# Kernel tuning notes

Measured on AMD Instinct MI355X. Metric: run time of the kernel, lower is better.

Reference implementation:

```python
import jax, jax.numpy as jnp
import numpy as np

N_NODES = 100000
NUM_LAYER = 3
REG_WEIGHT = 1e-4


def setup_inputs() -> dict:
    key = jax.random.key(0)
    ks = jax.random.split(key, 6)
    E = 1280000
    B = 4096
    D = 64
    # xavier-uniform-like scale for embedding table
    emb_weight = jax.random.normal(ks[0], (N_NODES, D), dtype=jnp.float32) * 0.01
    src = jax.random.randint(ks[1], (E,), 0, N_NODES, dtype=jnp.int32)
    dst = jax.random.randint(ks[2], (E,), 0, N_NODES, dtype=jnp.int32)
    users = jax.random.randint(ks[3], (B,), 0, N_NODES, dtype=jnp.int32)
    pos = jax.random.randint(ks[4], (B,), 0, N_NODES, dtype=jnp.int32)
    neg = jax.random.randint(ks[5], (B,), 0, N_NODES, dtype=jnp.int32)
    return {"emb_weight": emb_weight, "src": src, "dst": dst,
            "users": users, "pos": pos, "neg": neg}


def _edge_norm(src, dst):
    # DGL norm(): d = sum of edge mask (ones) per dst node; adj_e = d[src]^-0.5 * d[dst]^-0.5
    ones = jnp.ones(src.shape[0], dtype=jnp.float32)
    deg = jax.ops.segment_sum(ones, dst, num_segments=N_NODES)
    dinv = jnp.where(deg > 0, deg ** -0.5, 0.0)  # inf -> 0 handling
    return dinv[src] * dinv[dst]  # [E]


def _propagate(emb_weight, src, dst, adj):
    # LightGCN propagation: h_{l+1}[v] = sum_{(u->v)} adj_e * h_l[u]
    h = emb_weight
    layers = [h]
    for _ in range(NUM_LAYER):
        m = h[src] * adj[:, None]                    # [E, D] gather + edge weight
        h = jax.ops.segment_sum(m, dst, num_segments=N_NODES)  # [N, D] scatter-sum
        layers.append(h)
    return jnp.mean(jnp.stack(layers, axis=1), axis=1)  # mean over L+1 layers


def reference(emb_weight, src, dst, users, pos, neg):
    adj = _edge_norm(src, dst)
    all_emb = _propagate(emb_weight, src, dst, adj)

    u_e, p_e, n_e = all_emb[users], all_emb[pos], all_emb[neg]
    u0, p0, n0 = emb_weight[users], emb_weight[pos], emb_weight[neg]

    B = users.shape[0]
    reg_loss = 0.5 * (jnp.sum(u0 ** 2) + jnp.sum(p0 ** 2) + jnp.sum(n0 ** 2)) / B
    reg_loss = reg_loss * REG_WEIGHT

    pos_scores = jnp.sum(u_e * p_e, axis=1)
    neg_scores = jnp.sum(u_e * n_e, axis=1)
    loss_emb = jnp.mean(jax.nn.softplus(neg_scores - pos_scores))

    loss = loss_emb + reg_loss
    return loss, loss_emb, reg_loss
```

## Files before the change

### kernel.cpp

```cpp
#include <hip/hip_runtime.h>
#include <hip/hip_fp8.h>
#include <math.h>

#define N_NODES 100000
#define DIM 64
#define NUM_LAYER 3
#define BATCH 4096
#define REG_WEIGHT 1e-4f
#define NBUCKET 391
#define STAGE_CAP 4096
#define CURPAD 16
#define H_SCALE 64.0f
#define H_INV_SCALE (1.0f / 64.0f)

typedef float floatx2 __attribute__((ext_vector_type(2)));

__device__ unsigned char g_hf8[2][(size_t)N_NODES * DIM];
__device__ float g_sums[(size_t)3 * BATCH * DIM];
__device__ int   g_row_ptr[N_NODES + 1];
__device__ float g_dinv[N_NODES];
__device__ int   g_bcur[NBUCKET * CURPAD];
__device__ unsigned int g_stage[NBUCKET * STAGE_CAP];
__device__ int   g_csr[1280000];
__device__ int   g_shead[N_NODES];
__device__ int   g_snext[3 * BATCH];
__device__ float g_part_sp[BATCH];
__device__ float g_part_rg[BATCH];

__device__ inline void fma4_fp8(unsigned int d, float w,
                                float& a0, float& a1, float& a2, float& a3) {
    floatx2 lo = __builtin_amdgcn_cvt_pk_f32_fp8((int)d, false);
    floatx2 hi = __builtin_amdgcn_cvt_pk_f32_fp8((int)d, true);
    a0 = fmaf(w, lo.x, a0); a1 = fmaf(w, lo.y, a1);
    a2 = fmaf(w, hi.x, a2); a3 = fmaf(w, hi.y, a3);
}
__device__ inline unsigned int pack4_fp8(float a0, float a1, float a2, float a3) {
    int w = __builtin_amdgcn_cvt_pk_fp8_f32(a0, a1, 0, false);
    w     = __builtin_amdgcn_cvt_pk_fp8_f32(a2, a3, w, true);
    return (unsigned int)w;
}

#define EDGES_PER_THREAD 8
__global__ void __launch_bounds__(1024) stage_buckets(const int* __restrict__ src,
                                                      const int* __restrict__ dst, int E,
                                                      const int* __restrict__ users,
                                                      const int* __restrict__ pos,
                                                      const int* __restrict__ neg,
                                                      const float* __restrict__ emb) {
    __shared__ int h[NBUCKET];
    __shared__ int cur[NBUCKET];
    int tid = threadIdx.x;
    int gt = blockIdx.x * 1024 + tid;
    if (gt < 3 * BATCH) {
        int which = gt / BATCH, s = gt - which * BATCH;
        const int* idx = (which == 0) ? users : ((which == 1) ? pos : neg);
        g_snext[gt] = atomicExch(&g_shead[idx[s]], gt + 1);
    }
    int base = blockIdx.x * (1024 * EDGES_PER_THREAD);
    for (int i = tid; i < NBUCKET; i += 1024) h[i] = 0;
    __syncthreads();
    int myd[EDGES_PER_THREAD], mys[EDGES_PER_THREAD];
    #pragma unroll
    for (int k = 0; k < EDGES_PER_THREAD; ++k) {
        int e = base + k * 1024 + tid;
        if (e < E) {
            myd[k] = dst[e]; mys[k] = src[e];
            atomicAdd(&h[myd[k] >> 8], 1);
        } else myd[k] = -1;
    }
    __syncthreads();
    for (int i = tid; i < NBUCKET; i += 1024) {
        int c = h[i];
        cur[i] = c ? (atomicAdd(&g_bcur[i * CURPAD], c) + i * STAGE_CAP) : 0;
    }
    __syncthreads();
    #pragma unroll
    for (int k = 0; k < EDGES_PER_THREAD; ++k) {
        if (myd[k] >= 0) {
            int p = atomicAdd(&cur[myd[k] >> 8], 1);
            g_stage[p] = (unsigned int)((mys[k] << 8) | (myd[k] & 255));
        }
    }
    {
        const int NW = N_NODES * DIM / 4;
        int stride = gridDim.x * 1024;
        unsigned int* hw = (unsigned int*)g_hf8[0];
        for (int k = blockIdx.x * 1024 + tid; k < NW; k += stride) {
            const float* e = emb + (size_t)k * 4;
            hw[k] = pack4_fp8(e[0] * H_SCALE, e[1] * H_SCALE,
                              e[2] * H_SCALE, e[3] * H_SCALE);
        }
    }
}

__global__ void __launch_bounds__(512) finalize_place() {
    __shared__ int cs[512];
    __shared__ int lh[256], sc[256], cur[256];
    int b = blockIdx.x, t = threadIdx.x;
    int c = (t < NBUCKET) ? g_bcur[t * CURPAD] : 0;
    cs[t] = c;
    __syncthreads();
    for (int off = 1; off < 512; off <<= 1) {
        int x = (t >= off) ? cs[t - off] : 0;
        __syncthreads();
        cs[t] += x;
        __syncthreads();
    }
    int mybase = (b > 0) ? cs[b - 1] : 0;
    int cnt    = cs[b] - mybase;
    if (b == 0 && t == 0) g_row_ptr[N_NODES] = cs[NBUCKET - 1];
    int sbeg = b * STAGE_CAP;
    if (t < 256) lh[t] = 0;
    __syncthreads();
    for (int k = t; k < cnt; k += 512)
        atomicAdd(&lh[g_stage[sbeg + k] & 255], 1);
    __syncthreads();
    int v = 0;
    if (t < 256) { v = lh[t]; sc[t] = v; }
    __syncthreads();
    for (int off = 1; off < 256; off <<= 1) {
        int x = (t >= off && t < 256) ? sc[t - off] : 0;
        __syncthreads();
        if (t < 256) sc[t] += x;
        __syncthreads();
    }
    if (t < 256) {
        int start = mybase + sc[t] - v;
        cur[t] = start;
        int node = (b << 8) + t;
        if (node < N_NODES) {
            g_row_ptr[node] = start;
            g_dinv[node]    = (v > 0) ? rsqrtf((float)v) : 0.0f;
        }
    }
    __syncthreads();
    for (int k = t; k < cnt; k += 512) {
        unsigned int e = g_stage[sbeg + k];
        int pos = atomicAdd(&cur[e & 255], 1);
        g_csr[pos] = (int)(e >> 8);
    }
}

__global__ void pull_layer_fp8(const unsigned char* __restrict__ h,
                               unsigned char* __restrict__ hn, int do_gather) {
    int gid0 = blockIdx.x * blockDim.x + threadIdx.x;
    if (do_gather && gid0 < NBUCKET) g_bcur[gid0 * CURPAD] = 0;
    int wid  = gid0 >> 6;
    int lane = threadIdx.x & 63;
    int nA = wid * 2, nB = nA + 1;
    if (nA >= N_NODES) return;
    bool hasB = (nB < N_NODES);
    int g  = lane >> 4;
    int li = lane & 15;
    int begA = g_row_ptr[nA], endA = g_row_ptr[nA + 1];
    int begB = hasB ? g_row_ptr[nB] : 0, endB = hasB ? g_row_ptr[nB + 1] : 0;
    float dinvA = g_dinv[nA];
    float dinvB = hasB ? g_dinv[nB] : 0.0f;
    int lenA = endA - begA, lenB = endB - begB;
    int maxLen = max(lenA, lenB);
    float aA0 = 0.f, aA1 = 0.f, aA2 = 0.f, aA3 = 0.f;
    float aB0 = 0.f, aB1 = 0.f, aB2 = 0.f, aB3 = 0.f;
    for (int off = 0; off < maxLen; off += 64) {
        int kA = off + lane;
        int sA = 0; float wA = 0.0f;
        if (kA < lenA) { sA = g_csr[begA + kA]; wA = g_dinv[sA] * dinvA; }
        int sB = 0; float wB = 0.0f;
        if (kA < lenB) { sB = g_csr[begB + kA]; wB = g_dinv[sB] * dinvB; }
        int cnt = min(64, maxLen - off);
        for (int j = 0; j < cnt; j += 16) {
            int   sA1 = __shfl(sA, j + g),      sA2 = __shfl(sA, j + 4 + g);
            int   sA3 = __shfl(sA, j + 8 + g),  sA4 = __shfl(sA, j + 12 + g);
            int   sB1 = __shfl(sB, j + g),      sB2 = __shfl(sB, j + 4 + g);
            int   sB3 = __shfl(sB, j + 8 + g),  sB4 = __shfl(sB, j + 12 + g);
            float wA1 = __shfl(wA, j + g),      wA2 = __shfl(wA, j + 4 + g);
            float wA3 = __shfl(wA, j + 8 + g),  wA4 = __shfl(wA, j + 12 + g);
            float wB1 = __shfl(wB, j + g),      wB2 = __shfl(wB, j + 4 + g);
            float wB3 = __shfl(wB, j + 8 + g),  wB4 = __shfl(wB, j + 12 + g);
            unsigned int dA1 = *(const unsigned int*)(h + (size_t)sA1 * DIM + li * 4);
            unsigned int dA2 = *(const unsigned int*)(h + (size_t)sA2 * DIM + li * 4);
            unsigned int dA3 = *(const unsigned int*)(h + (size_t)sA3 * DIM + li * 4);
            unsigned int dA4 = *(const unsigned int*)(h + (size_t)sA4 * DIM + li * 4);
            unsigned int dB1 = *(const unsigned int*)(h + (size_t)sB1 * DIM + li * 4);
            unsigned int dB2 = *(const unsigned int*)(h + (size_t)sB2 * DIM + li * 4);
            unsigned int dB3 = *(const unsigned int*)(h + (size_t)sB3 * DIM + li * 4);
            unsigned int dB4 = *(const unsigned int*)(h + (size_t)sB4 * DIM + li * 4);
            fma4_fp8(dA1, wA1, aA0, aA1, aA2, aA3);
            fma4_fp8(dA2, wA2, aA0, aA1, aA2, aA3);
            fma4_fp8(dA3, wA3, aA0, aA1, aA2, aA3);
            fma4_fp8(dA4, wA4, aA0, aA1, aA2, aA3);
            fma4_fp8(dB1, wB1, aB0, aB1, aB2, aB3);
            fma4_fp8(dB2, wB2, aB0, aB1, aB2, aB3);
            fma4_fp8(dB3, wB3, aB0, aB1, aB2, aB3);
            fma4_fp8(dB4, wB4, aB0, aB1, aB2, aB3);
        }
    }
    #pragma unroll
    for (int off = 16; off < 64; off <<= 1) {
        aA0 += __shfl_xor(aA0, off); aA1 += __shfl_xor(aA1, off);
        aA2 += __shfl_xor(aA2, off); aA3 += __shfl_xor(aA3, off);
        aB0 += __shfl_xor(aB0, off); aB1 += __shfl_xor(aB1, off);
        aB2 += __shfl_xor(aB2, off); aB3 += __shfl_xor(aB3, off);
    }
    if (lane < 16) {
        *(unsigned int*)(hn + (size_t)nA * DIM + li * 4) = pack4_fp8(aA0, aA1, aA2, aA3);
        if (hasB)
            *(unsigned int*)(hn + (size_t)nB * DIM + li * 4) = pack4_fp8(aB0, aB1, aB2, aB3);
    }
    if (do_gather) {
        int sidx = g_shead[nA];
        while (sidx > 0) {
            int sreal = sidx - 1;
            if (lane < 16) {
                float* sp = &g_sums[(size_t)sreal * DIM + li * 4];
                sp[0] = aA0 * H_INV_SCALE; sp[1] = aA1 * H_INV_SCALE;
                sp[2] = aA2 * H_INV_SCALE; sp[3] = aA3 * H_INV_SCALE;
            }
            sidx = g_snext[sreal];
        }
        if (lane == 0) g_shead[nA] = 0;
        if (hasB) {
            sidx = g_shead[nB];
            while (sidx > 0) {
                int sreal = sidx - 1;
                if (lane < 16) {
                    float* sp = &g_sums[(size_t)sreal * DIM + li * 4];
                    sp[0] = aB0 * H_INV_SCALE; sp[1] = aB1 * H_INV_SCALE;
                    sp[2] = aB2 * H_INV_SCALE; sp[3] = aB3 * H_INV_SCALE;
                }
                sidx = g_snext[sreal];
            }
            if (lane == 0) g_shead[nB] = 0;
        }
    }
}

__global__ void pull_sampled(const unsigned char* __restrict__ h,
                             const int* __restrict__ users, const int* __restrict__ pos,
                             const int* __restrict__ neg) {
    int wid  = (blockIdx.x * blockDim.x + threadIdx.x) >> 6;
    int lane = threadIdx.x & 63;
    if (wid >= 3 * BATCH) return;
    int which = wid / BATCH;
    int i     = wid - which * BATCH;
    const int* idx = (which == 0) ? users : ((which == 1) ? pos : neg);
    int node = idx[i];
    int g  = lane >> 4;
    int li = lane & 15;
    int beg = g_row_ptr[node], end = g_row_ptr[node + 1];
    float dinv_d = g_dinv[node];
    float a0 = 0.f, a1 = 0.f, a2 = 0.f, a3 = 0.f;
    for (int base = beg; base < end; base += 64) {
        int k = base + lane;
        int s = 0; float w = 0.0f;
        if (k < end) { s = g_csr[k]; w = g_dinv[s] * dinv_d; }
        int cnt = min(64, end - base);
        for (int j = 0; j < cnt; j += 16) {
            int   sA = __shfl(s, j + g),      sB = __shfl(s, j + 4 + g);
            int   sC = __shfl(s, j + 8 + g),  sD = __shfl(s, j + 12 + g);
            float wA = __shfl(w, j + g),      wB = __shfl(w, j + 4 + g);
            float wC = __shfl(w, j + 8 + g),  wD = __shfl(w, j + 12 + g);
            unsigned int dA = *(const unsigned int*)(h + (size_t)sA * DIM + li * 4);
            unsigned int dB = *(const unsigned int*)(h + (size_t)sB * DIM + li * 4);
            unsigned int dC = *(const unsigned int*)(h + (size_t)sC * DIM + li * 4);
            unsigned int dD = *(const unsigned int*)(h + (size_t)sD * DIM + li * 4);
            fma4_fp8(dA, wA, a0, a1, a2, a3);
            fma4_fp8(dB, wB, a0, a1, a2, a3);
            fma4_fp8(dC, wC, a0, a1, a2, a3);
            fma4_fp8(dD, wD, a0, a1, a2, a3);
        }
    }
    #pragma unroll
    for (int off = 16; off < 64; off <<= 1) {
        a0 += __shfl_xor(a0, off);
        a1 += __shfl_xor(a1, off);
        a2 += __shfl_xor(a2, off);
        a3 += __shfl_xor(a3, off);
    }
    if (lane < 16) {
        unsigned int dn = *(const unsigned int*)(h + (size_t)node * DIM + li * 4);
        floatx2 lo = __builtin_amdgcn_cvt_pk_f32_fp8((int)dn, false);
        floatx2 hi = __builtin_amdgcn_cvt_pk_f32_fp8((int)dn, true);
        float* sp = &g_sums[(size_t)wid * DIM + li * 4];
        sp[0] += (a0 + lo.x) * H_INV_SCALE;
        sp[1] += (a1 + lo.y) * H_INV_SCALE;
        sp[2] += (a2 + hi.x) * H_INV_SCALE;
        sp[3] += (a3 + hi.y) * H_INV_SCALE;
    }
}

__global__ void score_reduce(const float* __restrict__ emb,
                             const int* __restrict__ users, const int* __restrict__ pos,
                             const int* __restrict__ neg) {
    int wid  = (blockIdx.x * blockDim.x + threadIdx.x) >> 6;
    int lane = threadIdx.x & 63;
    if (wid >= BATCH) return;
    float u0 = emb[(size_t)users[wid] * DIM + lane];
    float p0 = emb[(size_t)pos[wid]   * DIM + lane];
    float n0 = emb[(size_t)neg[wid]   * DIM + lane];
    float u = 0.25f * (g_sums[(size_t)wid * DIM + lane] + u0);
    float p = 0.25f * (g_sums[(size_t)(BATCH + wid) * DIM + lane] + p0);
    float n = 0.25f * (g_sums[(size_t)(2 * BATCH + wid) * DIM + lane] + n0);
    float ps = u * p;
    float ns = u * n;
    float rg = u0 * u0 + p0 * p0 + n0 * n0;
    #pragma unroll
    for (int off = 32; off > 0; off >>= 1) {
        ps += __shfl_down(ps, off);
        ns += __shfl_down(ns, off);
        rg += __shfl_down(rg, off);
    }
    if (lane == 0) {
        float x  = ns - ps;
        float sp = fmaxf(x, 0.0f) + log1pf(expf(-fabsf(x)));
        g_part_sp[wid] = sp;
        g_part_rg[wid] = rg;
    }
}

__global__ void final_reduce(float* __restrict__ out) {
    __shared__ float s_sp[256], s_rg[256];
    int t = threadIdx.x;
    float sp = 0.0f, rg = 0.0f;
    for (int i = t; i < BATCH; i += 256) { sp += g_part_sp[i]; rg += g_part_rg[i]; }
    s_sp[t] = sp; s_rg[t] = rg;
    __syncthreads();
    for (int off = 128; off > 0; off >>= 1) {
        if (t < off) { s_sp[t] += s_sp[t + off]; s_rg[t] += s_rg[t + off]; }
        __syncthreads();
    }
    if (t == 0) {
        float loss_emb = s_sp[0] / (float)BATCH;
        float reg      = 0.5f * s_rg[0] / (float)BATCH * REG_WEIGHT;
        out[0] = loss_emb + reg;
        out[1] = loss_emb;
        out[2] = reg;
    }
}

extern "C" void kernel_launch(void* const* d_in, const int* in_sizes, int n_in,
                              void* d_out, int out_size, void* d_ws, size_t ws_size,
                              hipStream_t stream) {
    const float* emb   = (const float*)d_in[0];
    const int*   src   = (const int*)d_in[1];
    const int*   dst   = (const int*)d_in[2];
    const int*   users = (const int*)d_in[3];
    const int*   pos   = (const int*)d_in[4];
    const int*   neg   = (const int*)d_in[5];
    const int E = in_sizes[1];
    float* out = (float*)d_out;

    unsigned char* hf_a;  hipGetSymbolAddress((void**)&hf_a, HIP_SYMBOL(g_hf8));
    unsigned char* hf_b = hf_a + (size_t)N_NODES * DIM;

    const int STAGE_BLOCKS = (E + 1024 * EDGES_PER_THREAD - 1) / (1024 * EDGES_PER_THREAD);
    stage_buckets<<<STAGE_BLOCKS, 1024, 0, stream>>>(src, dst, E, users, pos, neg, emb);
    finalize_place<<<NBUCKET, 512, 0, stream>>>();

    const int NPAIR = (N_NODES + 1) / 2;
    const int PULL_BLOCKS = (NPAIR * 64 + 255) / 256;

    pull_layer_fp8<<<PULL_BLOCKS, 256, 0, stream>>>(hf_a, hf_b, 1);

    pull_layer_fp8<<<PULL_BLOCKS, 256, 0, stream>>>(hf_b, hf_a, 0);

    pull_sampled<<<(3 * BATCH * 64 + 255) / 256, 256, 0, stream>>>(hf_a, users, pos, neg);

    score_reduce<<<(BATCH * 64 + 255) / 256, 256, 0, stream>>>(emb, users, pos, neg);
    final_reduce<<<1, 256, 0, stream>>>(out);
}
```

Measured before the change: 192.6 us.

## Pack source index with dinv into CSR and assign one node per quarter-wave

Adds a pass that builds an int2 CSR holding each source index next to its degree-inverse-sqrt, so the pull kernels no longer make a dependent gather into g_dinv per edge. The pull kernels now give each 16-lane quarter-wave its own destination node and walk its edges four at a time, replacing the cooperative index load, shuffles and cross-group xor reduction. This cuts shuffle and reduction overhead and idle lanes for low-degree nodes. In exchange it costs an extra kernel launch, a 10 MB int2 array to write and read, and more sequential per-node edge loops that each load redundant clamped entries.

Result: faster. 187.4 us (-2.7%).

```diff
diff --git a/kernel.cpp b/kernel.cpp
--- a/kernel.cpp
+++ b/kernel.cpp
@@ -22,6 +22,7 @@
 __device__ int   g_bcur[NBUCKET * CURPAD];
 __device__ unsigned int g_stage[NBUCKET * STAGE_CAP];
 __device__ int   g_csr[1280000];
+__device__ int2  g_csr2[1280000];
 __device__ int   g_shead[N_NODES];
 __device__ int   g_snext[3 * BATCH];
 __device__ float g_part_sp[BATCH];
@@ -141,151 +142,108 @@
     }
 }
 
+__global__ void build_wcsr(int E) {
+    int i = blockIdx.x * blockDim.x + threadIdx.x;
+    if (i < E) {
+        int s = g_csr[i];
+        g_csr2[i] = make_int2(s, __float_as_int(g_dinv[s]));
+    }
+}
+
 __global__ void pull_layer_fp8(const unsigned char* __restrict__ h,
                                unsigned char* __restrict__ hn, int do_gather) {
     int gid0 = blockIdx.x * blockDim.x + threadIdx.x;
     if (do_gather && gid0 < NBUCKET) g_bcur[gid0 * CURPAD] = 0;
     int wid  = gid0 >> 6;
     int lane = threadIdx.x & 63;
-    int nA = wid * 2, nB = nA + 1;
-    if (nA >= N_NODES) return;
-    bool hasB = (nB < N_NODES);
     int g  = lane >> 4;
     int li = lane & 15;
-    int begA = g_row_ptr[nA], endA = g_row_ptr[nA + 1];
-    int begB = hasB ? g_row_ptr[nB] : 0, endB = hasB ? g_row_ptr[nB + 1] : 0;
-    float dinvA = g_dinv[nA];
-    float dinvB = hasB ? g_dinv[nB] : 0.0f;
-    int lenA = endA - begA, lenB = endB - begB;
-    int maxLen = max(lenA, lenB);
-    float aA0 = 0.f, aA1 = 0.f, aA2 = 0.f, aA3 = 0.f;
-    float aB0 = 0.f, aB1 = 0.f, aB2 = 0.f, aB3 = 0.f;
-    for (int off = 0; off < maxLen; off += 64) {
-        int kA = off + lane;
-        int sA = 0; float wA = 0.0f;
-        if (kA < lenA) { sA = g_csr[begA + kA]; wA = g_dinv[sA] * dinvA; }
-        int sB = 0; float wB = 0.0f;
-        if (kA < lenB) { sB = g_csr[begB + kA]; wB = g_dinv[sB] * dinvB; }
-        int cnt = min(64, maxLen - off);
-        for (int j = 0; j < cnt; j += 16) {
-            int   sA1 = __shfl(sA, j + g),      sA2 = __shfl(sA, j + 4 + g);
-            int   sA3 = __shfl(sA, j + 8 + g),  sA4 = __shfl(sA, j + 12 + g);
-            int   sB1 = __shfl(sB, j + g),      sB2 = __shfl(sB, j + 4 + g);
-            int   sB3 = __shfl(sB, j + 8 + g),  sB4 = __shfl(sB, j + 12 + g);
-            float wA1 = __shfl(wA, j + g),      wA2 = __shfl(wA, j + 4 + g);
-            float wA3 = __shfl(wA, j + 8 + g),  wA4 = __shfl(wA, j + 12 + g);
-            float wB1 = __shfl(wB, j + g),      wB2 = __shfl(wB, j + 4 + g);
-            float wB3 = __shfl(wB, j + 8 + g),  wB4 = __shfl(wB, j + 12 + g);
-            unsigned int dA1 = *(const unsigned int*)(h + (size_t)sA1 * DIM + li * 4);
-            unsigned int dA2 = *(const unsigned int*)(h + (size_t)sA2 * DIM + li * 4);
-            unsigned int dA3 = *(const unsigned int*)(h + (size_t)sA3 * DIM + li * 4);
-            unsigned int dA4 = *(const unsigned int*)(h + (size_t)sA4 * DIM + li * 4);
-            unsigned int dB1 = *(const unsigned int*)(h + (size_t)sB1 * DIM + li * 4);
-            unsigned int dB2 = *(const unsigned int*)(h + (size_t)sB2 * DIM + li * 4);
-            unsigned int dB3 = *(const unsigned int*)(h + (size_t)sB3 * DIM + li * 4);
-            unsigned int dB4 = *(const unsigned int*)(h + (size_t)sB4 * DIM + li * 4);
-            fma4_fp8(dA1, wA1, aA0, aA1, aA2, aA3);
-            fma4_fp8(dA2, wA2, aA0, aA1, aA2, aA3);
-            fma4_fp8(dA3, wA3, aA0, aA1, aA2, aA3);
-            fma4_fp8(dA4, wA4, aA0, aA1, aA2, aA3);
-            fma4_fp8(dB1, wB1, aB0, aB1, aB2, aB3);
-            fma4_fp8(dB2, wB2, aB0, aB1, aB2, aB3);
-            fma4_fp8(dB3, wB3, aB0, aB1, aB2, aB3);
-            fma4_fp8(dB4, wB4, aB0, aB1, aB2, aB3);
+    int n = wid * 4 + g;
+    if (n >= N_NODES) return;
+    int beg = g_row_ptr[n], end = g_row_ptr[n + 1];
+    float dinvN = g_dinv[n];
+    float a0 = 0.f, a1 = 0.f, a2 = 0.f, a3 = 0.f;
+    for (int k = beg; k < end; k += 4) {
+        int k1 = min(k + 1, end - 1);
+        int k2 = min(k + 2, end - 1);
+        int k3 = min(k + 3, end - 1);
+        int2 e0 = g_csr2[k];
+        int2 e1 = g_csr2[k1];
+        int2 e2 = g_csr2[k2];
+        int2 e3 = g_csr2[k3];
+        unsigned int d0 = *(const unsigned int*)(h + (size_t)e0.x * DIM + li * 4);
+        unsigned int d1 = *(const unsigned int*)(h + (size_t)e1.x * DIM + li * 4);
+        unsigned int d2 = *(const unsigned int*)(h + (size_t)e2.x * DIM + li * 4);
+        unsigned int d3 = *(const unsigned int*)(h + (size_t)e3.x * DIM + li * 4);
+        float w0 = __int_as_float(e0.y) * dinvN;
+        float w1 = (k + 1 < end) ? __int_as_float(e1.y) * dinvN : 0.0f;
+        float w2 = (k + 2 < end) ? __int_as_float(e2.y) * dinvN : 0.0f;
+        float w3 = (k + 3 < end) ? __int_as_float(e3.y) * dinvN : 0.0f;
+        fma4_fp8(d0, w0, a0, a1, a2, a3);
+        fma4_fp8(d1, w1, a0, a1, a2, a3);
+        fma4_fp8(d2, w2, a0, a1, a2, a3);
+        fma4_fp8(d3, w3, a0, a1, a2, a3);
+    }
+    *(unsigned int*)(hn + (size_t)n * DIM + li * 4) = pack4_fp8(a0, a1, a2, a3);
+    if (do_gather) {
+        int sidx = g_shead[n];
+        while (sidx > 0) {
+            int sr = sidx - 1;
+            float* sp = &g_sums[(size_t)sr * DIM + li * 4];
+            sp[0] = a0 * H_INV_SCALE; sp[1] = a1 * H_INV_SCALE;
+            sp[2] = a2 * H_INV_SCALE; sp[3] = a3 * H_INV_SCALE;
+            sidx = g_snext[sr];
         }
-    }
-    #pragma unroll
-    for (int off = 16; off < 64; off <<= 1) {
-        aA0 += __shfl_xor(aA0, off); aA1 += __shfl_xor(aA1, off);
-        aA2 += __shfl_xor(aA2, off); aA3 += __shfl_xor(aA3, off);
-        aB0 += __shfl_xor(aB0, off); aB1 += __shfl_xor(aB1, off);
-        aB2 += __shfl_xor(aB2, off); aB3 += __shfl_xor(aB3, off);
-    }
-    if (lane < 16) {
-        *(unsigned int*)(hn + (size_t)nA * DIM + li * 4) = pack4_fp8(aA0, aA1, aA2, aA3);
-        if (hasB)
-            *(unsigned int*)(hn + (size_t)nB * DIM + li * 4) = pack4_fp8(aB0, aB1, aB2, aB3);
-    }
-    if (do_gather) {
-        int sidx = g_shead[nA];
-        while (sidx > 0) {
-            int sreal = sidx - 1;
-            if (lane < 16) {
-                float* sp = &g_sums[(size_t)sreal * DIM + li * 4];
-                sp[0] = aA0 * H_INV_SCALE; sp[1] = aA1 * H_INV_SCALE;
-                sp[2] = aA2 * H_INV_SCALE; sp[3] = aA3 * H_INV_SCALE;
-            }
-            sidx = g_snext[sreal];
-        }
-        if (lane == 0) g_shead[nA] = 0;
-        if (hasB) {
-            sidx = g_shead[nB];
-            while (sidx > 0) {
-                int sreal = sidx - 1;
-                if (lane < 16) {
-                    float* sp = &g_sums[(size_t)sreal * DIM + li * 4];
-                    sp[0] = aB0 * H_INV_SCALE; sp[1] = aB1 * H_INV_SCALE;
-                    sp[2] = aB2 * H_INV_SCALE; sp[3] = aB3 * H_INV_SCALE;
-                }
-                sidx = g_snext[sreal];
-            }
-            if (lane == 0) g_shead[nB] = 0;
-        }
+        if (li == 0) g_shead[n] = 0;
     }
 }
 
 __global__ void pull_sampled(const unsigned char* __restrict__ h,
                              const int* __restrict__ users, const int* __restrict__ pos,
                              const int* __restrict__ neg) {
-    int wid  = (blockIdx.x * blockDim.x + threadIdx.x) >> 6;
+    int gid0 = blockIdx.x * blockDim.x + threadIdx.x;
+    int wid  = gid0 >> 6;
     int lane = threadIdx.x & 63;
-    if (wid >= 3 * BATCH) return;
-    int which = wid / BATCH;
-    int i     = wid - which * BATCH;
+    int g  = lane >> 4;
+    int li = lane & 15;
+    int s = wid * 4 + g;
+    if (s >= 3 * BATCH) return;
+    int which = s >> 12;
+    int i     = s & (BATCH - 1);
     const int* idx = (which == 0) ? users : ((which == 1) ? pos : neg);
     int node = idx[i];
-    int g  = lane >> 4;
-    int li = lane & 15;
     int beg = g_row_ptr[node], end = g_row_ptr[node + 1];
-    float dinv_d = g_dinv[node];
+    float dinvN = g_dinv[node];
     float a0 = 0.f, a1 = 0.f, a2 = 0.f, a3 = 0.f;
-    for (int base = beg; base < end; base += 64) {
-        int k = base + lane;
-        int s = 0; float w = 0.0f;
-        if (k < end) { s = g_csr[k]; w = g_dinv[s] * dinv_d; }
-        int cnt = min(64, end - base);
-        for (int j = 0; j < cnt; j += 16) {
-            int   sA = __shfl(s, j + g),      sB = __shfl(s, j + 4 + g);
-            int   sC = __shfl(s, j + 8 + g),  sD = __shfl(s, j + 12 + g);
-            float wA = __shfl(w, j + g),      wB = __shfl(w, j + 4 + g);
-            float wC = __shfl(w, j + 8 + g),  wD = __shfl(w, j + 12 + g);
-            unsigned int dA = *(const unsigned int*)(h + (size_t)sA * DIM + li * 4);
-            unsigned int dB = *(const unsigned int*)(h + (size_t)sB * DIM + li * 4);
-            unsigned int dC = *(const unsigned int*)(h + (size_t)sC * DIM + li * 4);
-            unsigned int dD = *(const unsigned int*)(h + (size_t)sD * DIM + li * 4);
-            fma4_fp8(dA, wA, a0, a1, a2, a3);
-            fma4_fp8(dB, wB, a0, a1, a2, a3);
-            fma4_fp8(dC, wC, a0, a1, a2, a3);
-            fma4_fp8(dD, wD, a0, a1, a2, a3);
-        }
-    }
-    #pragma unroll
-    for (int off = 16; off < 64; off <<= 1) {
-        a0 += __shfl_xor(a0, off);
-        a1 += __shfl_xor(a1, off);
-        a2 += __shfl_xor(a2, off);
-        a3 += __shfl_xor(a3, off);
-    }
-    if (lane < 16) {
-        unsigned int dn = *(const unsigned int*)(h + (size_t)node * DIM + li * 4);
-        floatx2 lo = __builtin_amdgcn_cvt_pk_f32_fp8((int)dn, false);
-        floatx2 hi = __builtin_amdgcn_cvt_pk_f32_fp8((int)dn, true);
-        float* sp = &g_sums[(size_t)wid * DIM + li * 4];
-        sp[0] += (a0 + lo.x) * H_INV_SCALE;
-        sp[1] += (a1 + lo.y) * H_INV_SCALE;
-        sp[2] += (a2 + hi.x) * H_INV_SCALE;
-        sp[3] += (a3 + hi.y) * H_INV_SCALE;
-    }
+    for (int k = beg; k < end; k += 4) {
+        int k1 = min(k + 1, end - 1);
+        int k2 = min(k + 2, end - 1);
+        int k3 = min(k + 3, end - 1);
+        int2 e0 = g_csr2[k];
+        int2 e1 = g_csr2[k1];
+        int2 e2 = g_csr2[k2];
+        int2 e3 = g_csr2[k3];
+        unsigned int d0 = *(const unsigned int*)(h + (size_t)e0.x * DIM + li * 4);
+        unsigned int d1 = *(const unsigned int*)(h + (size_t)e1.x * DIM + li * 4);
+        unsigned int d2 = *(const unsigned int*)(h + (size_t)e2.x * DIM + li * 4);
+        unsigned int d3 = *(const unsigned int*)(h + (size_t)e3.x * DIM + li * 4);
+        float w0 = __int_as_float(e0.y) * dinvN;
+        float w1 = (k + 1 < end) ? __int_as_float(e1.y) * dinvN : 0.0f;
+        float w2 = (k + 2 < end) ? __int_as_float(e2.y) * dinvN : 0.0f;
+        float w3 = (k + 3 < end) ? __int_as_float(e3.y) * dinvN : 0.0f;
+        fma4_fp8(d0, w0, a0, a1, a2, a3);
+        fma4_fp8(d1, w1, a0, a1, a2, a3);
+        fma4_fp8(d2, w2, a0, a1, a2, a3);
+        fma4_fp8(d3, w3, a0, a1, a2, a3);
+    }
+    unsigned int dn = *(const unsigned int*)(h + (size_t)node * DIM + li * 4);
+    floatx2 lo = __builtin_amdgcn_cvt_pk_f32_fp8((int)dn, false);
+    floatx2 hi = __builtin_amdgcn_cvt_pk_f32_fp8((int)dn, true);
+    float* sp = &g_sums[(size_t)s * DIM + li * 4];
+    sp[0] += (a0 + lo.x) * H_INV_SCALE;
+    sp[1] += (a1 + lo.y) * H_INV_SCALE;
+    sp[2] += (a2 + hi.x) * H_INV_SCALE;
+    sp[3] += (a3 + hi.y) * H_INV_SCALE;
 }
 
 __global__ void score_reduce(const float* __restrict__ emb,
@@ -355,15 +313,17 @@
     const int STAGE_BLOCKS = (E + 1024 * EDGES_PER_THREAD - 1) / (1024 * EDGES_PER_THREAD);
     stage_buckets<<<STAGE_BLOCKS, 1024, 0, stream>>>(src, dst, E, users, pos, neg, emb);
     finalize_place<<<NBUCKET, 512, 0, stream>>>();
-
-    const int NPAIR = (N_NODES + 1) / 2;
-    const int PULL_BLOCKS = (NPAIR * 64 + 255) / 256;
+    build_wcsr<<<(E + 255) / 256, 256, 0, stream>>>(E);
+
+    const int NQUAD = (N_NODES + 3) / 4;
+    const int PULL_BLOCKS = (NQUAD * 64 + 255) / 256;
 
     pull_layer_fp8<<<PULL_BLOCKS, 256, 0, stream>>>(hf_a, hf_b, 1);
 
     pull_layer_fp8<<<PULL_BLOCKS, 256, 0, stream>>>(hf_b, hf_a, 0);
 
-    pull_sampled<<<(3 * BATCH * 64 + 255) / 256, 256, 0, stream>>>(hf_a, users, pos, neg);
+    const int SAMP_BLOCKS = ((3 * BATCH + 3) / 4 * 64 + 255) / 256;
+    pull_sampled<<<SAMP_BLOCKS, 256, 0, stream>>>(hf_a, users, pos, neg);
 
     score_reduce<<<(BATCH * 64 + 255) / 256, 256, 0, stream>>>(emb, users, pos, neg);
     final_reduce<<<1, 256, 0, stream>>>(out);
```
